# Kernel tuning notes

Hardware: AMD Instinct MI355X
Metric: run time of the kernel (lower is better)

Reference implementation:

```python
import jax, jax.numpy as jnp
import numpy as np

N_NODE = 4095
D_EMB = 32
D_MODEL = 64
NHEADS = 8
ALPHA = 1.0
B = N_NODE + 1  # batch must equal n_node+1 (see einsum 'nm,tmd->tnd')
T = 32


def setup_inputs() -> dict:
    key = jax.random.key(0)
    ks = jax.random.split(key, 16)
    f32 = jnp.float32
    inp = {
        "q": jax.random.normal(ks[0], (B, T, D_MODEL), f32),
        "k": jax.random.normal(ks[1], (B, T, D_MODEL), f32),
        "v": jax.random.normal(ks[2], (B, T, D_MODEL), f32),
        # learned parameters (torch init is randn; scaled for numeric stability)
        "emb": jax.random.normal(ks[3], (N_NODE + 1, D_EMB), f32) * 0.05,
        "We": jax.random.normal(ks[4], (D_EMB, D_MODEL, D_MODEL), f32) * 0.05,
        "be": jax.random.normal(ks[5], (D_EMB, D_MODEL), f32) * 0.05,
        "Wq": jax.random.normal(ks[6], (D_MODEL, D_MODEL), f32) * 0.05,
        "bq": jax.random.normal(ks[7], (D_MODEL,), f32) * 0.05,
        "Wk": jax.random.normal(ks[8], (D_MODEL, D_MODEL), f32) * 0.05,
        "bk": jax.random.normal(ks[9], (D_MODEL,), f32) * 0.05,
        "Wv": jax.random.normal(ks[10], (D_MODEL, D_MODEL), f32) * 0.05,
        "bv": jax.random.normal(ks[11], (D_MODEL,), f32) * 0.05,
        "Wo": jax.random.normal(ks[12], (D_MODEL, D_MODEL), f32) * 0.05,
        "bo": jax.random.normal(ks[13], (D_MODEL,), f32) * 0.05,
    }
    return inp


def _elu(x, alpha):
    return jnp.where(x > 0, x, alpha * (jnp.exp(x) - 1.0))


def _split_heads(x, h):
    # torch.cat(torch.split(x, D//h, dim=-1), dim=0): [B,T,D] -> [h*B,T,D/h]
    b, t, d = x.shape
    return jnp.moveaxis(x.reshape(b, t, h, d // h), 2, 0).reshape(h * b, t, d // h)


def _merge_heads(x, b, h):
    # torch.cat(torch.split(x, B, dim=0), dim=-1): [h*B,T,D/h] -> [B,T,D]
    hb, t, dh = x.shape
    return jnp.moveaxis(x.reshape(h, b, t, dh), 0, 2).reshape(b, t, h * dh)


def reference(q, k, v, emb, We, be, Wq, bq, Wk, bk, Wv, bv, Wo, bo):
    Bq, Tq, D = q.shape
    h = NHEADS
    scale = (D // h) ** 0.5

    # linear projections (torch Linear: x @ W.T + b)
    q = q @ Wq.T + bq
    k = k @ Wk.T + bk
    v = v @ Wv.T + bv

    # adjacency: sum over d_emb of pairwise diff == s_i - s_j (same math, no [N,N,E] tensor)
    s = jnp.sum(emb, axis=-1)  # [N+1]
    sim = s[:, None] - s[None, :]  # [N+1, N+1]
    A = jax.nn.softmax(_elu(sim, ALPHA), axis=-1) + jnp.eye(Bq, dtype=q.dtype)

    # updateQ: adjacency-weighted diffusion + per-node weight matrices
    qt = jnp.transpose(q, (1, 0, 2))  # [T, N, D]
    W = jnp.einsum('ne,eio->nio', emb, We)  # [N, D, D]
    b = emb @ be  # [N, D]
    q_ = jnp.einsum('nm,tmd->tnd', A, qt)  # diffusion
    q_ = jnp.einsum('tnd,ndo->tno', q_, W) + b  # per-node matmul
    q = jnp.transpose(q_, (1, 0, 2))  # [N, T, D]

    # manual multi-head attention via split/cat
    qh = _split_heads(q, h)
    kh = _split_heads(k, h)
    vh = _split_heads(v, h)
    attn = jax.nn.softmax(jnp.einsum('btd,bsd->bts', qh, kh) / scale, axis=-1)
    out = jnp.einsum('bts,bsd->btd', attn, vh)
    out = _merge_heads(out, Bq, h)
    return out @ Wo.T + bo
```

## Files before the change

### kernel.cpp

```cpp
#include <hip/hip_runtime.h>
#include <hip/hip_bf16.h>

constexpr int NN  = 4096;
constexpr int DE  = 32;
constexpr int TD  = 2048;

typedef __attribute__((ext_vector_type(8))) short short8;
typedef __attribute__((ext_vector_type(4))) float f32x4;

#define MFMA16(a, b, c) __builtin_amdgcn_mfma_f32_16x16x32_bf16(a, b, c, 0, 0, 0)

__device__ inline ushort f2b(float x) {
    __hip_bfloat16 h = __float2bfloat16(x);
    union { __hip_bfloat16 h; ushort u; } c; c.h = h;
    return c.u;
}

__device__ inline float b2f(ushort u) {
    union { unsigned u; float f; } c; c.u = ((unsigned)u) << 16;
    return c.f;
}

__device__ inline short8 pack8(float4 a, float4 b) {
    short8 v;
    v[0] = (short)f2b(a.x); v[1] = (short)f2b(a.y); v[2] = (short)f2b(a.z); v[3] = (short)f2b(a.w);
    v[4] = (short)f2b(b.x); v[5] = (short)f2b(b.y); v[6] = (short)f2b(b.z); v[7] = (short)f2b(b.w);
    return v;
}

__device__ inline short8 pack8v(f32x4 a, f32x4 b) {
    short8 v;
    v[0] = (short)f2b(a[0]); v[1] = (short)f2b(a[1]); v[2] = (short)f2b(a[2]); v[3] = (short)f2b(a[3]);
    v[4] = (short)f2b(b[0]); v[5] = (short)f2b(b[1]); v[6] = (short)f2b(b[2]); v[7] = (short)f2b(b[3]);
    return v;
}

__device__ __forceinline__ short8 as_s8(f32x4 v) {
    union { f32x4 f; short8 s; } u; u.f = v; return u.s;
}

template<int OFF>
__device__ __forceinline__ f32x4 gl16(unsigned long long addr) {
    f32x4 d;
    asm volatile("global_load_dwordx4 %0, %1, off offset:%c2"
                 : "=v"(d) : "v"(addr), "n"(OFF) : "memory");
    return d;
}

__global__ __launch_bounds__(256) void k_prep(const float* __restrict__ emb,
                                              const float* __restrict__ We,
                                              const float* __restrict__ be,
                                              const float* __restrict__ Wk,
                                              const float* __restrict__ Wv,
                                              const float* __restrict__ Wo,
                                              float* __restrict__ s_g,
                                              ushort* __restrict__ embbf,
                                              ushort* __restrict__ WeTT,
                                              ushort* __restrict__ Wkbf,
                                              ushort* __restrict__ Wvbf,
                                              ushort* __restrict__ Wobf,
                                              float* __restrict__ bn) {
    int id = blockIdx.x, tid = threadIdx.x;
    if (id < 16) {
        int n = id * 256 + tid;
        const float4* e4 = (const float4*)(emb + n * DE);
        float s = 0.f;
#pragma unroll
        for (int i = 0; i < DE / 4; ++i) { float4 v = e4[i]; s += v.x + v.y + v.z + v.w; }
        s_g[n] = s;
    } else if (id < 144) {
        int g4 = (id - 16) * 256 + tid;
        float4 v = *(const float4*)&emb[(size_t)g4 * 4];
        ushort4 o; o.x = f2b(v.x); o.y = f2b(v.y); o.z = f2b(v.z); o.w = f2b(v.w);
        *(ushort4*)&embbf[(size_t)g4 * 4] = o;
    } else if (id < 656) {
        int gid = (id - 144) * 256 + tid;
        int od = gid >> 5, e = gid & 31;
        int o = od >> 6, d = od & 63;
        WeTT[gid] = f2b(We[(size_t)e * 4096 + d * 64 + o]);
    } else if (id < 704) {
        int id5 = id - 656;
        int which = id5 >> 4, gid = (id5 & 15) * 256 + tid;
        const float* src = which == 0 ? Wk : (which == 1 ? Wv : Wo);
        ushort* dst = which == 0 ? Wkbf : (which == 1 ? Wvbf : Wobf);
        dst[gid] = f2b(src[gid]);
    } else {
        int gid = (id - 704) * 256 + tid;
        int n = gid >> 6, o = gid & 63;
        float acc = 0.f;
#pragma unroll
        for (int e = 0; e < DE; ++e) acc += emb[n * DE + e] * be[e * 64 + o];
        bn[gid] = acc;
    }
}

__global__ __launch_bounds__(256) void k_pr(const float* __restrict__ X,
                                            const float* __restrict__ W,
                                            const float* __restrict__ bias,
                                            ushort* __restrict__ Y,
                                            const float* __restrict__ s_g,
                                            int* __restrict__ perm) {
    __shared__ float ss[NN];
    int id = blockIdx.x, tid = threadIdx.x;
    if (id < 512) {
        int lane = tid & 63, wid = tid >> 6;
        int r0 = id * 256 + wid * 64;
        int l15 = lane & 15, kb = lane >> 4;
        f32x4 acc[4][4] = {};
#pragma unroll
        for (int kk = 0; kk < 2; ++kk) {
            short8 af[4], bf[4];
#pragma unroll
            for (int f = 0; f < 4; ++f) {
                const float* ap = X + (size_t)(r0 + f * 16 + l15) * 64 + kk * 32 + kb * 8;
                af[f] = pack8(*(const float4*)ap, *(const float4*)(ap + 4));
                const float* bp = W + (size_t)(f * 16 + l15) * 64 + kk * 32 + kb * 8;
                bf[f] = pack8(*(const float4*)bp, *(const float4*)(bp + 4));
            }
#pragma unroll
            for (int i = 0; i < 4; ++i)
#pragma unroll
                for (int j = 0; j < 4; ++j)
                    acc[i][j] = MFMA16(af[i], bf[j], acc[i][j]);
        }
        float bcol[4];
#pragma unroll
        for (int j = 0; j < 4; ++j) bcol[j] = bias[j * 16 + l15];
#pragma unroll
        for (int i = 0; i < 4; ++i)
#pragma unroll
            for (int j = 0; j < 4; ++j)
#pragma unroll
                for (int r = 0; r < 4; ++r)
                    Y[(size_t)(r0 + i * 16 + kb * 4 + r) * 64 + j * 16 + l15] =
                        f2b(acc[i][j][r] + bcol[j]);
    } else {
        for (int i = tid; i < NN; i += 256) ss[i] = s_g[i];
        __syncthreads();
        int g = tid >> 5, l = tid & 31;
        int n = (id - 512) * 8 + g;
        float sn = ss[n];
        int cnt = 0;
        for (int j2 = 0; j2 < 128; ++j2) {
            int m = j2 * 32 + l;
            float sm = ss[m];
            cnt += (sm < sn) || (sm == sn && m < n);
        }
        for (int off = 16; off; off >>= 1) cnt += __shfl_down(cnt, off, 32);
        if (l == 0) perm[cnt] = n;
    }
}

__global__ __launch_bounds__(256) void k_csum(const ushort* __restrict__ qp,
                                              const float* __restrict__ s_g,
                                              const int* __restrict__ perm,
                                              float* __restrict__ Cj,
                                              float* __restrict__ Cb) {
    __shared__ int ns[64];
    __shared__ float bs[64];
    int bx = blockIdx.x, by = blockIdx.y, tid = threadIdx.x;
    if (tid < 64) {
        int n = perm[bx * 64 + tid];
        ns[tid] = n;
        bs[tid] = __expf(-s_g[n]);
    }
    __syncthreads();
    int j = by * 256 + tid;
    float run[8] = {};
    for (int ii = 0; ii < 64; ++ii) {
        float qv = b2f(qp[(size_t)ns[ii] * 2048 + j]);
        float b = bs[ii], t = qv;
#pragma unroll
        for (int k2 = 0; k2 < 8; ++k2) { run[k2] += t; t *= b; }
    }
    float* cp = Cj + ((size_t)bx * 2048 + j) * 8;
    *(float4*)cp       = make_float4(run[0], run[1], run[2], run[3]);
    *(float4*)(cp + 4) = make_float4(run[4], run[5], run[6], run[7]);
    if (by == 0 && tid < 64) {
        float b = bs[tid], bk = 1.f;
#pragma unroll
        for (int k2 = 0; k2 < 8; ++k2) {
            float v = bk;
            for (int off = 32; off; off >>= 1) v += __shfl_down(v, off, 64);
            if (tid == 0) Cb[bx * 8 + k2] = v;
            bk *= b;
        }
    }
}

__global__ __launch_bounds__(256) void k_pre(const float* __restrict__ Cj,
                                             float* __restrict__ PRE,
                                             const float* __restrict__ Cb,
                                             float* __restrict__ CbPre) {
    __shared__ float sCb[512];
    int tid = threadIdx.x;
    if (blockIdx.x < 64) {
        int gid = blockIdx.x * 256 + tid;
        float run = 0.f;
        for (int c = 0; c < 64; ++c) {
            PRE[(size_t)c * 16384 + gid] = run;
            run += Cj[(size_t)c * 16384 + gid];
        }
        PRE[(size_t)64 * 16384 + gid] = run;
    } else {
        sCb[tid] = Cb[tid];
        sCb[tid + 256] = Cb[tid + 256];
        __syncthreads();
        if (tid < 8) {
            float run = 0.f;
            for (int c = 0; c < 64; ++c) {
                CbPre[c * 8 + tid] = run;
                run += sCb[c * 8 + tid];
            }
            CbPre[512 + tid] = run;
        }
    }
}

__global__ __launch_bounds__(256) void k_combw(const ushort* __restrict__ qp,
                                               const float* __restrict__ s_g,
                                               const int* __restrict__ perm,
                                               const float* __restrict__ PRE,
                                               const float* __restrict__ CbPre,
                                               ushort* __restrict__ qdifb,
                                               const ushort* __restrict__ embbf,
                                               const ushort* __restrict__ WeTT,
                                               ushort* __restrict__ WnT) {
    __shared__ int ns[64];
    __shared__ float sa[64], sb[64];
    int id = blockIdx.x, tid = threadIdx.x;
    if (id < 512) {
        int bx = id & 63, by = id >> 6;
        if (tid < 64) {
            int n = perm[bx * 64 + tid];
            ns[tid] = n;
            float s = s_g[n];
            sa[tid] = __expf(s);
            sb[tid] = __expf(-s);
        }
        __syncthreads();
        int j = by * 256 + tid;
        float T[8], pre[8];
        {
            const float* pp = PRE + (size_t)bx * 16384 + (size_t)j * 8;
            float4 u0 = *(const float4*)pp, u1 = *(const float4*)(pp + 4);
            pre[0] = u0.x; pre[1] = u0.y; pre[2] = u0.z; pre[3] = u0.w;
            pre[4] = u1.x; pre[5] = u1.y; pre[6] = u1.z; pre[7] = u1.w;
            const float* tp = PRE + (size_t)64 * 16384 + (size_t)j * 8;
            float4 t0 = *(const float4*)tp, t1 = *(const float4*)(tp + 4);
            T[0] = t0.x; T[1] = t0.y; T[2] = t0.z; T[3] = t0.w;
            T[4] = t1.x; T[5] = t1.y; T[6] = t1.z; T[7] = t1.w;
        }
        float TB[8], preb[8];
        {
            float4 v0 = *(const float4*)&CbPre[bx * 8], v1 = *(const float4*)&CbPre[bx * 8 + 4];
            preb[0] = v0.x; preb[1] = v0.y; preb[2] = v0.z; preb[3] = v0.w;
            preb[4] = v1.x; preb[5] = v1.y; preb[6] = v1.z; preb[7] = v1.w;
            float4 t0 = *(const float4*)&CbPre[512], t1 = *(const float4*)&CbPre[516];
            TB[0] = t0.x; TB[1] = t0.y; TB[2] = t0.z; TB[3] = t0.w;
            TB[4] = t1.x; TB[5] = t1.y; TB[6] = t1.z; TB[7] = t1.w;
        }
        for (int ii = 0; ii < 64; ++ii) {
            int n = ns[ii];
            float a = sa[ii], b = sb[ii];
            float g0 = 0.36787944117144233f;
            float g1 = g0 * a;
            float g2 = g1 * a * 0.5f;
            float g3 = g2 * a * (1.f / 3.f);
            float g4 = g3 * a * 0.25f;
            float g5 = g4 * a * 0.2f;
            float g6 = g5 * a * (1.f / 6.f);
            float g7 = g6 * a * (1.f / 7.f);
            float Z = a * preb[1]
                    + g0 * (TB[0] - preb[0]) + g1 * (TB[1] - preb[1])
                    + g2 * (TB[2] - preb[2]) + g3 * (TB[3] - preb[3])
                    + g4 * (TB[4] - preb[4]) + g5 * (TB[5] - preb[5])
                    + g6 * (TB[6] - preb[6]) + g7 * (TB[7] - preb[7]);
            float izv = 1.f / Z;
            float qv = b2f(qp[(size_t)n * 2048 + j]);
            float ss2 = g0 * (T[0] - pre[0]) + g1 * (T[1] - pre[1])
                      + g2 * (T[2] - pre[2]) + g3 * (T[3] - pre[3])
                      + g4 * (T[4] - pre[4]) + g5 * (T[5] - pre[5])
                      + g6 * (T[6] - pre[6]) + g7 * (T[7] - pre[7]);
            float outv = (a * pre[1] + ss2) * izv + qv;
            qdifb[(size_t)n * 2048 + j] = f2b(outv);
            float bk = 1.f;
#pragma unroll
            for (int k2 = 0; k2 < 8; ++k2) { pre[k2] += bk * qv; preb[k2] += bk; bk *= b; }
        }
    } else {
        int w2 = id - 512;
        int lane = tid & 63, wid = tid >> 6;
        int n0  = (w2 & 31) * 128 + (wid >> 1) * 64;
        int od0 = (w2 >> 5) * 128 + (wid & 1) * 64;
        int l15 = lane & 15, kb = lane >> 4;
        short8 af[4], bf[4];
#pragma unroll
        for (int f = 0; f < 4; ++f) {
            af[f] = *(const short8*)(embbf + (size_t)(n0 + f * 16 + l15) * 32 + kb * 8);
            bf[f] = *(const short8*)(WeTT + (size_t)(od0 + f * 16 + l15) * 32 + kb * 8);
        }
        f32x4 acc[4][4] = {};
#pragma unroll
        for (int i = 0; i < 4; ++i)
#pragma unroll
            for (int j = 0; j < 4; ++j)
                acc[i][j] = MFMA16(af[i], bf[j], acc[i][j]);
#pragma unroll
        for (int i = 0; i < 4; ++i)
#pragma unroll
            for (int j = 0; j < 4; ++j)
#pragma unroll
                for (int r = 0; r < 4; ++r)
                    WnT[(size_t)(n0 + i * 16 + kb * 4 + r) * 4096 + od0 + j * 16 + l15] =
                        f2b(acc[i][j][r]);
    }
}

__global__ __launch_bounds__(128, 2) void k_fused(const float* __restrict__ kin,
                                                  const float* __restrict__ vin,
                                                  const ushort* __restrict__ qdifb,
                                                  const ushort* __restrict__ WnT,
                                                  const float* __restrict__ bn,
                                                  const ushort* __restrict__ Wkbf,
                                                  const float* __restrict__ bk,
                                                  const ushort* __restrict__ Wvbf,
                                                  const float* __restrict__ bv,
                                                  const ushort* __restrict__ Wobf,
                                                  const float* __restrict__ bo,
                                                  float* __restrict__ out) {
    __shared__ ushort Kb[2][544];
    __shared__ ushort Qb[2][544];
    __shared__ ushort Vb[2][640];
    __shared__ ushort Pb[2][1280];
    __shared__ ushort attb[2][32 * 72];
    int tid = threadIdx.x, lane = tid & 63, w = tid >> 6;
    int b = blockIdx.x * 2 + w;
    int l15 = lane & 15, g = lane >> 4;

    unsigned long long ka = (unsigned long long)(kin   + (size_t)b * TD   + (8 + l15) * 64 + g * 8);
    unsigned long long va = (unsigned long long)(vin   + (size_t)b * TD   + (8 + l15) * 64 + g * 8);
    unsigned long long qa = (unsigned long long)(qdifb + (size_t)b * TD   + (8 + l15) * 64 + g * 8);
    unsigned long long wa = (unsigned long long)(WnT   + (size_t)b * 4096 + (24 + l15) * 64 + g * 8);
    f32x4 k00a = gl16<-2048>(ka), k00b = gl16<-2032>(ka);
    f32x4 k01a = gl16<-1920>(ka), k01b = gl16<-1904>(ka);
    f32x4 k10a = gl16< 2048>(ka), k10b = gl16< 2064>(ka);
    f32x4 k11a = gl16< 2176>(ka), k11b = gl16< 2192>(ka);
    f32x4 v00a = gl16<-2048>(va), v00b = gl16<-2032>(va);
    f32x4 v01a = gl16<-1920>(va), v01b = gl16<-1904>(va);
    f32x4 v10a = gl16< 2048>(va), v10b = gl16< 2064>(va);
    f32x4 v11a = gl16< 2176>(va), v11b = gl16< 2192>(va);
    f32x4 q00 = gl16<-1024>(qa), q01 = gl16<-960>(qa);
    f32x4 q10 = gl16< 1024>(qa), q11 = gl16<1088>(qa);
    f32x4 w00 = gl16<-3072>(wa), w01 = gl16<-3008>(wa);
    f32x4 w10 = gl16<-1024>(wa), w11 = gl16< -960>(wa);
    f32x4 w20 = gl16< 1024>(wa), w21 = gl16< 1088>(wa);
    f32x4 w30 = gl16< 3072>(wa), w31 = gl16< 3136>(wa);

    float bkc[4], bvc[4], bnc[4], boc[4];
#pragma unroll
    for (int j = 0; j < 4; ++j) {
        bkc[j] = bk[j * 16 + l15];
        bvc[j] = bv[j * 16 + l15];
        bnc[j] = bn[b * 64 + j * 16 + l15];
        boc[j] = bo[j * 16 + l15];
    }

    asm volatile("s_waitcnt vmcnt(0)" ::: "memory");
    __builtin_amdgcn_sched_barrier(0);

    short8 kaf[2][2], vaf[2][2], qaf[2][2], bqf[4][2];
    kaf[0][0] = pack8v(k00a, k00b); kaf[1][0] = pack8v(k01a, k01b);
    kaf[0][1] = pack8v(k10a, k10b); kaf[1][1] = pack8v(k11a, k11b);
    vaf[0][0] = pack8v(v00a, v00b); vaf[1][0] = pack8v(v01a, v01b);
    vaf[0][1] = pack8v(v10a, v10b); vaf[1][1] = pack8v(v11a, v11b);
    qaf[0][0] = as_s8(q00); qaf[1][0] = as_s8(q01);
    qaf[0][1] = as_s8(q10); qaf[1][1] = as_s8(q11);
    bqf[0][0] = as_s8(w00); bqf[0][1] = as_s8(w01);
    bqf[1][0] = as_s8(w10); bqf[1][1] = as_s8(w11);
    bqf[2][0] = as_s8(w20); bqf[2][1] = as_s8(w21);
    bqf[3][0] = as_s8(w30); bqf[3][1] = as_s8(w31);

    const float SCALE = 0.35355339059327373f;
    short8 zfrag = {};
    int hh_w = l15 >> 3, d1_w = l15 & 7;

#pragma unroll
    for (int j = 0; j < 4; ++j) {
        f32x4 ak[2] = {}, aq[2] = {}, av[2] = {};
#pragma unroll
        for (int kk = 0; kk < 2; ++kk) {
            short8 bkfj = *(const short8*)(Wkbf + (size_t)(j * 16 + l15) * 64 + kk * 32 + g * 8);
            short8 bvfj = *(const short8*)(Wvbf + (size_t)(j * 16 + l15) * 64 + kk * 32 + g * 8);
#pragma unroll
            for (int ti = 0; ti < 2; ++ti) {
                ak[ti] = MFMA16(kaf[kk][ti], bkfj, ak[ti]);
                aq[ti] = MFMA16(qaf[kk][ti], bqf[j][kk], aq[ti]);
                av[ti] = MFMA16(vaf[kk][ti], bvfj, av[ti]);
            }
        }
#pragma unroll
        for (int ti = 0; ti < 2; ++ti) {
#pragma unroll
            for (int r = 0; r < 4; ++r) {
                int s = ti * 16 + g * 4 + r;
                Kb[w][hh_w * 272 + s * 8 + d1_w] = f2b(ak[ti][r] + bkc[j]);
                Qb[w][hh_w * 272 + s * 8 + d1_w] = f2b(aq[ti][r] + bnc[j]);
            }
#pragma unroll
            for (int r = 0; r < 4; r += 2) {
                int s = ti * 16 + g * 4 + r;
                ushort2 p; p.x = f2b(av[ti][r] + bvc[j]); p.y = f2b(av[ti][r + 1] + bvc[j]);
                *(ushort2*)&Vb[w][hh_w * 320 + d1_w * 40 + s] = p;
            }
        }
#pragma unroll
        for (int hh = 0; hh < 2; ++hh) {
            int h = j * 2 + hh;
            short8 kf[2], qf[2];
#pragma unroll
            for (int si = 0; si < 2; ++si)
                kf[si] = (lane < 16) ? *(const short8*)&Kb[w][hh * 272 + (si * 16 + l15) * 8] : zfrag;
#pragma unroll
            for (int ti = 0; ti < 2; ++ti)
                qf[ti] = (lane < 16) ? *(const short8*)&Qb[w][hh * 272 + (ti * 16 + l15) * 8] : zfrag;
            f32x4 sc[2][2];
#pragma unroll
            for (int si = 0; si < 2; ++si)
#pragma unroll
                for (int ti = 0; ti < 2; ++ti)
                    sc[si][ti] = MFMA16(kf[si], qf[ti], f32x4{});
#pragma unroll
            for (int ti = 0; ti < 2; ++ti) {
                float e0[4], e1[4], sm = 0.f;
#pragma unroll
                for (int r = 0; r < 4; ++r) {
                    e0[r] = __expf(sc[0][ti][r] * SCALE);
                    e1[r] = __expf(sc[1][ti][r] * SCALE);
                    sm += e0[r] + e1[r];
                }
                sm += __shfl_xor(sm, 16);
                sm += __shfl_xor(sm, 32);
                float inv = 1.f / sm;
                int t = ti * 16 + l15;
                unsigned p00 = (unsigned)f2b(e0[0] * inv) | ((unsigned)f2b(e0[1] * inv) << 16);
                unsigned p01 = (unsigned)f2b(e0[2] * inv) | ((unsigned)f2b(e0[3] * inv) << 16);
                unsigned p10 = (unsigned)f2b(e1[0] * inv) | ((unsigned)f2b(e1[1] * inv) << 16);
                unsigned p11 = (unsigned)f2b(e1[2] * inv) | ((unsigned)f2b(e1[3] * inv) << 16);
                *(unsigned*)&Pb[w][t * 40 + g * 4]          = p00;
                *(unsigned*)&Pb[w][t * 40 + g * 4 + 2]      = p01;
                *(unsigned*)&Pb[w][t * 40 + 16 + g * 4]     = p10;
                *(unsigned*)&Pb[w][t * 40 + 16 + g * 4 + 2] = p11;
            }
            short8 vf = *(const short8*)&Vb[w][hh * 320 + (l15 & 7) * 40 + g * 8];
#pragma unroll
            for (int ti = 0; ti < 2; ++ti) {
                short8 af = *(const short8*)&Pb[w][(ti * 16 + l15) * 40 + g * 8];
                f32x4 pv = MFMA16(af, vf, f32x4{});
                if (l15 < 8) {
#pragma unroll
                    for (int r = 0; r < 4; ++r)
                        attb[w][(ti * 16 + g * 4 + r) * 72 + h * 8 + l15] = f2b(pv[r]);
                }
            }
        }
    }

    short8 aof[2][2];
#pragma unroll
    for (int kk = 0; kk < 2; ++kk)
#pragma unroll
        for (int ti = 0; ti < 2; ++ti)
            aof[kk][ti] = *(const short8*)&attb[w][(ti * 16 + l15) * 72 + kk * 32 + g * 8];
    f32x4 co[2][4] = {};
#pragma unroll
    for (int kk = 0; kk < 2; ++kk)
#pragma unroll
        for (int j = 0; j < 4; ++j) {
            short8 bf = *(const short8*)(Wobf + (size_t)(j * 16 + l15) * 64 + kk * 32 + g * 8);
#pragma unroll
            for (int ti = 0; ti < 2; ++ti)
                co[ti][j] = MFMA16(aof[kk][ti], bf, co[ti][j]);
        }
#pragma unroll
    for (int ti = 0; ti < 2; ++ti)
#pragma unroll
        for (int j = 0; j < 4; ++j)
#pragma unroll
            for (int r = 0; r < 4; ++r)
                out[(size_t)b * TD + (ti * 16 + g * 4 + r) * 64 + j * 16 + l15] =
                    co[ti][j][r] + boc[j];
}

extern "C" void kernel_launch(void* const* d_in, const int* in_sizes, int n_in,
                              void* d_out, int out_size, void* d_ws, size_t ws_size,
                              hipStream_t stream) {
    const float* q   = (const float*)d_in[0];
    const float* k   = (const float*)d_in[1];
    const float* v   = (const float*)d_in[2];
    const float* emb = (const float*)d_in[3];
    const float* We  = (const float*)d_in[4];
    const float* be  = (const float*)d_in[5];
    const float* Wq  = (const float*)d_in[6];
    const float* bq  = (const float*)d_in[7];
    const float* Wk  = (const float*)d_in[8];
    const float* bk  = (const float*)d_in[9];
    const float* Wv  = (const float*)d_in[10];
    const float* bv  = (const float*)d_in[11];
    const float* Wo  = (const float*)d_in[12];
    const float* bo  = (const float*)d_in[13];

    float* ws = (float*)d_ws;
    ushort* qp    = (ushort*)ws;
    ushort* WnT   = (ushort*)(ws + 4194304);
    ushort* qdifb = (ushort*)(ws + 12582912);
    float*  Cj    = ws + 16777216;
    float*  bn    = ws + 17825792;
    float*  s_g   = ws + 18087936;
    int*    perm  = (int*)(ws + 18092032);
    float*  Cb    = ws + 18096128;
    ushort* embbf = (ushort*)(ws + 18096640);
    ushort* WeTT  = (ushort*)(ws + 18162176);
    ushort* Wkbf  = (ushort*)(ws + 18227712);
    ushort* Wvbf  = (ushort*)(ws + 18229760);
    ushort* Wobf  = (ushort*)(ws + 18231808);
    float*  PRE   = ws + 18233856;
    float*  CbPre = ws + 19298816;
    float*  outp  = (float*)d_out;

    k_prep <<<1728, 256, 0, stream>>>(emb, We, be, Wk, Wv, Wo,
                                      s_g, embbf, WeTT, Wkbf, Wvbf, Wobf, bn);
    k_pr   <<<1024, 256, 0, stream>>>(q, Wq, bq, qp, s_g, perm);
    k_csum <<<dim3(64, 8), 256, 0, stream>>>(qp, s_g, perm, Cj, Cb);
    k_pre  <<<65, 256, 0, stream>>>(Cj, PRE, Cb, CbPre);
    k_combw<<<1536, 256, 0, stream>>>(qp, s_g, perm, PRE, CbPre, qdifb,
                                      embbf, WeTT, WnT);
    k_fused<<<2048, 128, 0, stream>>>(k, v, qdifb, WnT, bn,
                                      Wkbf, bk, Wvbf, bv, Wobf, bo, outp);
}
```

Before: 116.1 us.

## Stage loads in fused attention kernel with staged waits and full-head LDS buffers

The fused attention kernel now issues its global loads in stages: K and Wk first, then V and Wv, then Q and WnT, then Wo. Explicit vmcnt waits let each projection start while later loads are still in flight. All heads' K/Q/V are written to larger LDS buffers before the attention loop, instead of interleaving projection and attention per head pair. The We transpose in k_prep is reorganised to read coalesced float4 per embedding slice, using fewer blocks, and two loops get unroll pragmas. This costs more LDS per block, which may lower occupancy, and it relies on the hand-written waitcnt counts being correct.

Result: no change. 114.8 us (-1.1%).

```diff
diff --git a/kernel.cpp b/kernel.cpp
--- a/kernel.cpp
+++ b/kernel.cpp
@@ -46,6 +46,17 @@
                  : "=v"(d) : "v"(addr), "n"(OFF) : "memory");
     return d;
 }
+
+template<int OFF>
+__device__ __forceinline__ float gl4(unsigned long long addr) {
+    float d;
+    asm volatile("global_load_dword %0, %1, off offset:%c2"
+                 : "=v"(d) : "v"(addr), "n"(OFF) : "memory");
+    return d;
+}
+
+#define WAITV(N) asm volatile("s_waitcnt vmcnt(" #N ")" ::: "memory"); \
+                 __builtin_amdgcn_sched_barrier(0)
 
 __global__ __launch_bounds__(256) void k_prep(const float* __restrict__ emb,
                                               const float* __restrict__ We,
@@ -73,19 +84,28 @@
         float4 v = *(const float4*)&emb[(size_t)g4 * 4];
         ushort4 o; o.x = f2b(v.x); o.y = f2b(v.y); o.z = f2b(v.z); o.w = f2b(v.w);
         *(ushort4*)&embbf[(size_t)g4 * 4] = o;
-    } else if (id < 656) {
-        int gid = (id - 144) * 256 + tid;
-        int od = gid >> 5, e = gid & 31;
-        int o = od >> 6, d = od & 63;
-        WeTT[gid] = f2b(We[(size_t)e * 4096 + d * 64 + o]);
-    } else if (id < 704) {
-        int id5 = id - 656;
+    } else if (id < 176) {
+        int e = id - 144;
+#pragma unroll
+        for (int u = 0; u < 4; ++u) {
+            int idx0 = tid * 16 + u * 4;
+            float4 v = *(const float4*)&We[(size_t)e * 4096 + idx0];
+            float vv[4] = {v.x, v.y, v.z, v.w};
+#pragma unroll
+            for (int i = 0; i < 4; ++i) {
+                int idx = idx0 + i;
+                int o = idx & 63, d = idx >> 6;
+                WeTT[(size_t)(o * 64 + d) * 32 + e] = f2b(vv[i]);
+            }
+        }
+    } else if (id < 224) {
+        int id5 = id - 176;
         int which = id5 >> 4, gid = (id5 & 15) * 256 + tid;
         const float* src = which == 0 ? Wk : (which == 1 ? Wv : Wo);
         ushort* dst = which == 0 ? Wkbf : (which == 1 ? Wvbf : Wobf);
         dst[gid] = f2b(src[gid]);
     } else {
-        int gid = (id - 704) * 256 + tid;
+        int gid = (id - 224) * 256 + tid;
         int n = gid >> 6, o = gid & 63;
         float acc = 0.f;
 #pragma unroll
@@ -197,6 +217,7 @@
     if (blockIdx.x < 64) {
         int gid = blockIdx.x * 256 + tid;
         float run = 0.f;
+#pragma unroll 8
         for (int c = 0; c < 64; ++c) {
             PRE[(size_t)c * 16384 + gid] = run;
             run += Cj[(size_t)c * 16384 + gid];
@@ -260,6 +281,7 @@
             TB[0] = t0.x; TB[1] = t0.y; TB[2] = t0.z; TB[3] = t0.w;
             TB[4] = t1.x; TB[5] = t1.y; TB[6] = t1.z; TB[7] = t1.w;
         }
+#pragma unroll 2
         for (int ii = 0; ii < 64; ++ii) {
             int n = ns[ii];
             float a = sa[ii], b = sb[ii];
@@ -329,167 +351,226 @@
                                                   const ushort* __restrict__ Wobf,
                                                   const float* __restrict__ bo,
                                                   float* __restrict__ out) {
-    __shared__ ushort Kb[2][544];
-    __shared__ ushort Qb[2][544];
-    __shared__ ushort Vb[2][640];
+    __shared__ ushort Kb[2][2176];
+    __shared__ ushort Qb[2][2176];
+    __shared__ ushort Vb[2][2560];
     __shared__ ushort Pb[2][1280];
-    __shared__ ushort attb[2][32 * 72];
+    __shared__ ushort attb[2][2304];
     int tid = threadIdx.x, lane = tid & 63, w = tid >> 6;
     int b = blockIdx.x * 2 + w;
     int l15 = lane & 15, g = lane >> 4;
-
-    unsigned long long ka = (unsigned long long)(kin   + (size_t)b * TD   + (8 + l15) * 64 + g * 8);
-    unsigned long long va = (unsigned long long)(vin   + (size_t)b * TD   + (8 + l15) * 64 + g * 8);
-    unsigned long long qa = (unsigned long long)(qdifb + (size_t)b * TD   + (8 + l15) * 64 + g * 8);
-    unsigned long long wa = (unsigned long long)(WnT   + (size_t)b * 4096 + (24 + l15) * 64 + g * 8);
-    f32x4 k00a = gl16<-2048>(ka), k00b = gl16<-2032>(ka);
-    f32x4 k01a = gl16<-1920>(ka), k01b = gl16<-1904>(ka);
-    f32x4 k10a = gl16< 2048>(ka), k10b = gl16< 2064>(ka);
-    f32x4 k11a = gl16< 2176>(ka), k11b = gl16< 2192>(ka);
-    f32x4 v00a = gl16<-2048>(va), v00b = gl16<-2032>(va);
-    f32x4 v01a = gl16<-1920>(va), v01b = gl16<-1904>(va);
-    f32x4 v10a = gl16< 2048>(va), v10b = gl16< 2064>(va);
-    f32x4 v11a = gl16< 2176>(va), v11b = gl16< 2192>(va);
-    f32x4 q00 = gl16<-1024>(qa), q01 = gl16<-960>(qa);
-    f32x4 q10 = gl16< 1024>(qa), q11 = gl16<1088>(qa);
-    f32x4 w00 = gl16<-3072>(wa), w01 = gl16<-3008>(wa);
-    f32x4 w10 = gl16<-1024>(wa), w11 = gl16< -960>(wa);
-    f32x4 w20 = gl16< 1024>(wa), w21 = gl16< 1088>(wa);
-    f32x4 w30 = gl16< 3072>(wa), w31 = gl16< 3136>(wa);
-
-    float bkc[4], bvc[4], bnc[4], boc[4];
-#pragma unroll
-    for (int j = 0; j < 4; ++j) {
-        bkc[j] = bk[j * 16 + l15];
-        bvc[j] = bv[j * 16 + l15];
-        bnc[j] = bn[b * 64 + j * 16 + l15];
-        boc[j] = bo[j * 16 + l15];
-    }
-
-    asm volatile("s_waitcnt vmcnt(0)" ::: "memory");
-    __builtin_amdgcn_sched_barrier(0);
-
-    short8 kaf[2][2], vaf[2][2], qaf[2][2], bqf[4][2];
-    kaf[0][0] = pack8v(k00a, k00b); kaf[1][0] = pack8v(k01a, k01b);
-    kaf[0][1] = pack8v(k10a, k10b); kaf[1][1] = pack8v(k11a, k11b);
-    vaf[0][0] = pack8v(v00a, v00b); vaf[1][0] = pack8v(v01a, v01b);
-    vaf[0][1] = pack8v(v10a, v10b); vaf[1][1] = pack8v(v11a, v11b);
-    qaf[0][0] = as_s8(q00); qaf[1][0] = as_s8(q01);
-    qaf[0][1] = as_s8(q10); qaf[1][1] = as_s8(q11);
-    bqf[0][0] = as_s8(w00); bqf[0][1] = as_s8(w01);
-    bqf[1][0] = as_s8(w10); bqf[1][1] = as_s8(w11);
-    bqf[2][0] = as_s8(w20); bqf[2][1] = as_s8(w21);
-    bqf[3][0] = as_s8(w30); bqf[3][1] = as_s8(w31);
-
+    int hh_w = l15 >> 3, d1_w = l15 & 7;
     const float SCALE = 0.35355339059327373f;
     short8 zfrag = {};
-    int hh_w = l15 >> 3, d1_w = l15 & 7;
-
-#pragma unroll
-    for (int j = 0; j < 4; ++j) {
-        f32x4 ak[2] = {}, aq[2] = {}, av[2] = {};
-#pragma unroll
-        for (int kk = 0; kk < 2; ++kk) {
-            short8 bkfj = *(const short8*)(Wkbf + (size_t)(j * 16 + l15) * 64 + kk * 32 + g * 8);
-            short8 bvfj = *(const short8*)(Wvbf + (size_t)(j * 16 + l15) * 64 + kk * 32 + g * 8);
-#pragma unroll
-            for (int ti = 0; ti < 2; ++ti) {
-                ak[ti] = MFMA16(kaf[kk][ti], bkfj, ak[ti]);
-                aq[ti] = MFMA16(qaf[kk][ti], bqf[j][kk], aq[ti]);
-                av[ti] = MFMA16(vaf[kk][ti], bvfj, av[ti]);
+
+    unsigned long long bkA = (unsigned long long)(bk + 32 + l15);
+    unsigned long long bnA = (unsigned long long)(bn + (size_t)b * 64 + 32 + l15);
+    unsigned long long bvA = (unsigned long long)(bv + 32 + l15);
+    unsigned long long boA = (unsigned long long)(bo + 32 + l15);
+    unsigned long long wkA = (unsigned long long)((const char*)Wkbf + l15 * 128 + g * 16 + 3072);
+    unsigned long long kaA = (unsigned long long)(kin + (size_t)b * TD + (8 + l15) * 64 + g * 8);
+    unsigned long long wvA = (unsigned long long)((const char*)Wvbf + l15 * 128 + g * 16 + 3072);
+    unsigned long long vaA = (unsigned long long)(vin + (size_t)b * TD + (8 + l15) * 64 + g * 8);
+    unsigned long long qaA = (unsigned long long)(qdifb + (size_t)b * TD + (8 + l15) * 64 + g * 8);
+    unsigned long long waA = (unsigned long long)(WnT + (size_t)b * 4096 + (24 + l15) * 64 + g * 8);
+    unsigned long long woA = (unsigned long long)((const char*)Wobf + l15 * 128 + g * 16 + 3072);
+
+    float bkc[4], bnc[4], bvc[4], boc[4];
+    bkc[0] = gl4<-128>(bkA); bkc[1] = gl4<-64>(bkA); bkc[2] = gl4<0>(bkA); bkc[3] = gl4<64>(bkA);
+    bnc[0] = gl4<-128>(bnA); bnc[1] = gl4<-64>(bnA); bnc[2] = gl4<0>(bnA); bnc[3] = gl4<64>(bnA);
+    bvc[0] = gl4<-128>(bvA); bvc[1] = gl4<-64>(bvA); bvc[2] = gl4<0>(bvA); bvc[3] = gl4<64>(bvA);
+    boc[0] = gl4<-128>(boA); boc[1] = gl4<-64>(boA); boc[2] = gl4<0>(boA); boc[3] = gl4<64>(boA);
+    f32x4 wk00 = gl16<-3072>(wkA), wk01 = gl16<-3008>(wkA);
+    f32x4 wk10 = gl16<-1024>(wkA), wk11 = gl16< -960>(wkA);
+    f32x4 wk20 = gl16< 1024>(wkA), wk21 = gl16< 1088>(wkA);
+    f32x4 wk30 = gl16< 3072>(wkA), wk31 = gl16< 3136>(wkA);
+    f32x4 k00a = gl16<-2048>(kaA), k00b = gl16<-2032>(kaA);
+    f32x4 k01a = gl16<-1920>(kaA), k01b = gl16<-1904>(kaA);
+    f32x4 k10a = gl16< 2048>(kaA), k10b = gl16< 2064>(kaA);
+    f32x4 k11a = gl16< 2176>(kaA), k11b = gl16< 2192>(kaA);
+    f32x4 wv00 = gl16<-3072>(wvA), wv01 = gl16<-3008>(wvA);
+    f32x4 wv10 = gl16<-1024>(wvA), wv11 = gl16< -960>(wvA);
+    f32x4 wv20 = gl16< 1024>(wvA), wv21 = gl16< 1088>(wvA);
+    f32x4 wv30 = gl16< 3072>(wvA), wv31 = gl16< 3136>(wvA);
+    f32x4 v00a = gl16<-2048>(vaA), v00b = gl16<-2032>(vaA);
+    f32x4 v01a = gl16<-1920>(vaA), v01b = gl16<-1904>(vaA);
+    f32x4 v10a = gl16< 2048>(vaA), v10b = gl16< 2064>(vaA);
+    f32x4 v11a = gl16< 2176>(vaA), v11b = gl16< 2192>(vaA);
+
+    WAITV(16);
+    {
+        short8 kaf[2][2], wkf[4][2];
+        kaf[0][0] = pack8v(k00a, k00b); kaf[1][0] = pack8v(k01a, k01b);
+        kaf[0][1] = pack8v(k10a, k10b); kaf[1][1] = pack8v(k11a, k11b);
+        wkf[0][0] = as_s8(wk00); wkf[0][1] = as_s8(wk01);
+        wkf[1][0] = as_s8(wk10); wkf[1][1] = as_s8(wk11);
+        wkf[2][0] = as_s8(wk20); wkf[2][1] = as_s8(wk21);
+        wkf[3][0] = as_s8(wk30); wkf[3][1] = as_s8(wk31);
+#pragma unroll
+        for (int j = 0; j < 4; ++j) {
+            f32x4 ak[2] = {};
+#pragma unroll
+            for (int kk = 0; kk < 2; ++kk)
+#pragma unroll
+                for (int ti = 0; ti < 2; ++ti)
+                    ak[ti] = MFMA16(kaf[kk][ti], wkf[j][kk], ak[ti]);
+#pragma unroll
+            for (int ti = 0; ti < 2; ++ti)
+#pragma unroll
+                for (int r = 0; r < 4; ++r) {
+                    int s = ti * 16 + g * 4 + r;
+                    Kb[w][(j * 2 + hh_w) * 272 + s * 8 + d1_w] = f2b(ak[ti][r] + bkc[j]);
+                }
+        }
+    }
+
+    f32x4 q00 = gl16<-1024>(qaA), q01 = gl16<-960>(qaA);
+    f32x4 q10 = gl16< 1024>(qaA), q11 = gl16<1088>(qaA);
+    f32x4 w00 = gl16<-3072>(waA), w01 = gl16<-3008>(waA);
+    f32x4 w10 = gl16<-1024>(waA), w11 = gl16< -960>(waA);
+    f32x4 w20 = gl16< 1024>(waA), w21 = gl16< 1088>(waA);
+    f32x4 w30 = gl16< 3072>(waA), w31 = gl16< 3136>(waA);
+
+    WAITV(12);
+    {
+        short8 vaf[2][2], wvf[4][2];
+        vaf[0][0] = pack8v(v00a, v00b); vaf[1][0] = pack8v(v01a, v01b);
+        vaf[0][1] = pack8v(v10a, v10b); vaf[1][1] = pack8v(v11a, v11b);
+        wvf[0][0] = as_s8(wv00); wvf[0][1] = as_s8(wv01);
+        wvf[1][0] = as_s8(wv10); wvf[1][1] = as_s8(wv11);
+        wvf[2][0] = as_s8(wv20); wvf[2][1] = as_s8(wv21);
+        wvf[3][0] = as_s8(wv30); wvf[3][1] = as_s8(wv31);
+#pragma unroll
+        for (int j = 0; j < 4; ++j) {
+            f32x4 av[2] = {};
+#pragma unroll
+            for (int kk = 0; kk < 2; ++kk)
+#pragma unroll
+                for (int ti = 0; ti < 2; ++ti)
+                    av[ti] = MFMA16(vaf[kk][ti], wvf[j][kk], av[ti]);
+#pragma unroll
+            for (int ti = 0; ti < 2; ++ti)
+#pragma unroll
+                for (int r = 0; r < 4; r += 2) {
+                    int s = ti * 16 + g * 4 + r;
+                    ushort2 p; p.x = f2b(av[ti][r] + bvc[j]); p.y = f2b(av[ti][r + 1] + bvc[j]);
+                    *(ushort2*)&Vb[w][(j * 2 + hh_w) * 320 + d1_w * 40 + s] = p;
+                }
+        }
+    }
+
+    f32x4 wo00 = gl16<-3072>(woA), wo01 = gl16<-3008>(woA);
+    f32x4 wo10 = gl16<-1024>(woA), wo11 = gl16< -960>(woA);
+    f32x4 wo20 = gl16< 1024>(woA), wo21 = gl16< 1088>(woA);
+    f32x4 wo30 = gl16< 3072>(woA), wo31 = gl16< 3136>(woA);
+
+    WAITV(8);
+    {
+        short8 qaf[2][2], bqf[4][2];
+        qaf[0][0] = as_s8(q00); qaf[1][0] = as_s8(q01);
+        qaf[0][1] = as_s8(q10); qaf[1][1] = as_s8(q11);
+        bqf[0][0] = as_s8(w00); bqf[0][1] = as_s8(w01);
+        bqf[1][0] = as_s8(w10); bqf[1][1] = as_s8(w11);
+        bqf[2][0] = as_s8(w20); bqf[2][1] = as_s8(w21);
+        bqf[3][0] = as_s8(w30); bqf[3][1] = as_s8(w31);
+#pragma unroll
+        for (int j = 0; j < 4; ++j) {
+            f32x4 aq[2] = {};
+#pragma unroll
+            for (int kk = 0; kk < 2; ++kk)
+#pragma unroll
+                for (int ti = 0; ti < 2; ++ti)
+                    aq[ti] = MFMA16(qaf[kk][ti], bqf[j][kk], aq[ti]);
+#pragma unroll
+            for (int ti = 0; ti < 2; ++ti)
+#pragma unroll
+                for (int r = 0; r < 4; ++r) {
+                    int s = ti * 16 + g * 4 + r;
+                    Qb[w][(j * 2 + hh_w) * 272 + s * 8 + d1_w] = f2b(aq[ti][r] + bnc[j]);
+                }
+        }
+    }
+
+#pragma unroll
+    for (int h = 0; h < 8; ++h) {
+        short8 kf[2], qf[2];
+#pragma unroll
+        for (int si = 0; si < 2; ++si)
+            kf[si] = (lane < 16) ? *(const short8*)&Kb[w][h * 272 + (si * 16 + l15) * 8] : zfrag;
+#pragma unroll
+        for (int ti = 0; ti < 2; ++ti)
+            qf[ti] = (lane < 16) ? *(const short8*)&Qb[w][h * 272 + (ti * 16 + l15) * 8] : zfrag;
+        f32x4 sc[2][2];
+#pragma unroll
+        for (int si = 0; si < 2; ++si)
+#pragma unroll
+            for (int ti = 0; ti < 2; ++ti)
+                sc[si][ti] = MFMA16(kf[si], qf[ti], f32x4{});
+#pragma unroll
+        for (int ti = 0; ti < 2; ++ti) {
+            float e0[4], e1[4], sm = 0.f;
+#pragma unroll
+            for (int r = 0; r < 4; ++r) {
+                e0[r] = __expf(sc[0][ti][r] * SCALE);
+                e1[r] = __expf(sc[1][ti][r] * SCALE);
+                sm += e0[r] + e1[r];
             }
-        }
+            sm += __shfl_xor(sm, 16);
+            sm += __shfl_xor(sm, 32);
+            float inv = 1.f / sm;
+            int t = ti * 16 + l15;
+            unsigned p00 = (unsigned)f2b(e0[0] * inv) | ((unsigned)f2b(e0[1] * inv) << 16);
+            unsigned p01 = (unsigned)f2b(e0[2] * inv) | ((unsigned)f2b(e0[3] * inv) << 16);
+            unsigned p10 = (unsigned)f2b(e1[0] * inv) | ((unsigned)f2b(e1[1] * inv) << 16);
+            unsigned p11 = (unsigned)f2b(e1[2] * inv) | ((unsigned)f2b(e1[3] * inv) << 16);
+            *(unsigned*)&Pb[w][t * 40 + g * 4]          = p00;
+            *(unsigned*)&Pb[w][t * 40 + g * 4 + 2]      = p01;
+            *(unsigned*)&Pb[w][t * 40 + 16 + g * 4]     = p10;
+            *(unsigned*)&Pb[w][t * 40 + 16 + g * 4 + 2] = p11;
+        }
+        short8 vf = *(const short8*)&Vb[w][h * 320 + (l15 & 7) * 40 + g * 8];
 #pragma unroll
         for (int ti = 0; ti < 2; ++ti) {
-#pragma unroll
-            for (int r = 0; r < 4; ++r) {
-                int s = ti * 16 + g * 4 + r;
-                Kb[w][hh_w * 272 + s * 8 + d1_w] = f2b(ak[ti][r] + bkc[j]);
-                Qb[w][hh_w * 272 + s * 8 + d1_w] = f2b(aq[ti][r] + bnc[j]);
+            short8 af = *(const short8*)&Pb[w][(ti * 16 + l15) * 40 + g * 8];
+            f32x4 pv = MFMA16(af, vf, f32x4{});
+            if (l15 < 8) {
+#pragma unroll
+                for (int r = 0; r < 4; ++r)
+                    attb[w][(ti * 16 + g * 4 + r) * 72 + h * 8 + l15] = f2b(pv[r]);
             }
-#pragma unroll
-            for (int r = 0; r < 4; r += 2) {
-                int s = ti * 16 + g * 4 + r;
-                ushort2 p; p.x = f2b(av[ti][r] + bvc[j]); p.y = f2b(av[ti][r + 1] + bvc[j]);
-                *(ushort2*)&Vb[w][hh_w * 320 + d1_w * 40 + s] = p;
-            }
-        }
-#pragma unroll
-        for (int hh = 0; hh < 2; ++hh) {
-            int h = j * 2 + hh;
-            short8 kf[2], qf[2];
-#pragma unroll
-            for (int si = 0; si < 2; ++si)
-                kf[si] = (lane < 16) ? *(const short8*)&Kb[w][hh * 272 + (si * 16 + l15) * 8] : zfrag;
+        }
+    }
+
+    WAITV(0);
+    {
+        short8 wof[4][2];
+        wof[0][0] = as_s8(wo00); wof[0][1] = as_s8(wo01);
+        wof[1][0] = as_s8(wo10); wof[1][1] = as_s8(wo11);
+        wof[2][0] = as_s8(wo20); wof[2][1] = as_s8(wo21);
+        wof[3][0] = as_s8(wo30); wof[3][1] = as_s8(wo31);
+        short8 aof[2][2];
+#pragma unroll
+        for (int kk = 0; kk < 2; ++kk)
 #pragma unroll
             for (int ti = 0; ti < 2; ++ti)
-                qf[ti] = (lane < 16) ? *(const short8*)&Qb[w][hh * 272 + (ti * 16 + l15) * 8] : zfrag;
-            f32x4 sc[2][2];
-#pragma unroll
-            for (int si = 0; si < 2; ++si)
+                aof[kk][ti] = *(const short8*)&attb[w][(ti * 16 + l15) * 72 + kk * 32 + g * 8];
+        f32x4 co[2][4] = {};
+#pragma unroll
+        for (int kk = 0; kk < 2; ++kk)
+#pragma unroll
+            for (int j = 0; j < 4; ++j)
 #pragma unroll
                 for (int ti = 0; ti < 2; ++ti)
-                    sc[si][ti] = MFMA16(kf[si], qf[ti], f32x4{});
-#pragma unroll
-            for (int ti = 0; ti < 2; ++ti) {
-                float e0[4], e1[4], sm = 0.f;
-#pragma unroll
-                for (int r = 0; r < 4; ++r) {
-                    e0[r] = __expf(sc[0][ti][r] * SCALE);
-                    e1[r] = __expf(sc[1][ti][r] * SCALE);
-                    sm += e0[r] + e1[r];
-                }
-                sm += __shfl_xor(sm, 16);
-                sm += __shfl_xor(sm, 32);
-                float inv = 1.f / sm;
-                int t = ti * 16 + l15;
-                unsigned p00 = (unsigned)f2b(e0[0] * inv) | ((unsigned)f2b(e0[1] * inv) << 16);
-                unsigned p01 = (unsigned)f2b(e0[2] * inv) | ((unsigned)f2b(e0[3] * inv) << 16);
-                unsigned p10 = (unsigned)f2b(e1[0] * inv) | ((unsigned)f2b(e1[1] * inv) << 16);
-                unsigned p11 = (unsigned)f2b(e1[2] * inv) | ((unsigned)f2b(e1[3] * inv) << 16);
-                *(unsigned*)&Pb[w][t * 40 + g * 4]          = p00;
-                *(unsigned*)&Pb[w][t * 40 + g * 4 + 2]      = p01;
-                *(unsigned*)&Pb[w][t * 40 + 16 + g * 4]     = p10;
-                *(unsigned*)&Pb[w][t * 40 + 16 + g * 4 + 2] = p11;
-            }
-            short8 vf = *(const short8*)&Vb[w][hh * 320 + (l15 & 7) * 40 + g * 8];
-#pragma unroll
-            for (int ti = 0; ti < 2; ++ti) {
-                short8 af = *(const short8*)&Pb[w][(ti * 16 + l15) * 40 + g * 8];
-                f32x4 pv = MFMA16(af, vf, f32x4{});
-                if (l15 < 8) {
-#pragma unroll
-                    for (int r = 0; r < 4; ++r)
-                        attb[w][(ti * 16 + g * 4 + r) * 72 + h * 8 + l15] = f2b(pv[r]);
-                }
-            }
-        }
-    }
-
-    short8 aof[2][2];
-#pragma unroll
-    for (int kk = 0; kk < 2; ++kk)
+                    co[ti][j] = MFMA16(aof[kk][ti], wof[j][kk], co[ti][j]);
 #pragma unroll
         for (int ti = 0; ti < 2; ++ti)
-            aof[kk][ti] = *(const short8*)&attb[w][(ti * 16 + l15) * 72 + kk * 32 + g * 8];
-    f32x4 co[2][4] = {};
-#pragma unroll
-    for (int kk = 0; kk < 2; ++kk)
-#pragma unroll
-        for (int j = 0; j < 4; ++j) {
-            short8 bf = *(const short8*)(Wobf + (size_t)(j * 16 + l15) * 64 + kk * 32 + g * 8);
-#pragma unroll
-            for (int ti = 0; ti < 2; ++ti)
-                co[ti][j] = MFMA16(aof[kk][ti], bf, co[ti][j]);
-        }
-#pragma unroll
-    for (int ti = 0; ti < 2; ++ti)
-#pragma unroll
-        for (int j = 0; j < 4; ++j)
-#pragma unroll
-            for (int r = 0; r < 4; ++r)
-                out[(size_t)b * TD + (ti * 16 + g * 4 + r) * 64 + j * 16 + l15] =
-                    co[ti][j][r] + boc[j];
+#pragma unroll
+            for (int j = 0; j < 4; ++j)
+#pragma unroll
+                for (int r = 0; r < 4; ++r)
+                    out[(size_t)b * TD + (ti * 16 + g * 4 + r) * 64 + j * 16 + l15] =
+                        co[ti][j][r] + boc[j];
+    }
 }
 
 extern "C" void kernel_launch(void* const* d_in, const int* in_sizes, int n_in,
@@ -528,7 +609,7 @@
     float*  CbPre = ws + 19298816;
     float*  outp  = (float*)d_out;
 
-    k_prep <<<1728, 256, 0, stream>>>(emb, We, be, Wk, Wv, Wo,
+    k_prep <<<1248, 256, 0, stream>>>(emb, We, be, Wk, Wv, Wo,
                                       s_g, embbf, WeTT, Wkbf, Wvbf, Wobf, bn);
     k_pr   <<<1024, 256, 0, stream>>>(q, Wq, bq, qp, s_g, perm);
     k_csum <<<dim3(64, 8), 256, 0, stream>>>(qp, s_g, perm, Cj, Cb);
```
